# Kernel tuning notes

Measured on AMD Instinct MI355X. Metric: run time of the kernel, lower is better.

## Reference

```python
import jax, jax.numpy as jnp
import numpy as np

NUM_SEQS = 4
Q_LEN = 512          # new query tokens per sequence (chunked prefill)
SEQ_LEN = 2048       # total tokens per sequence (context + query)
NUM_Q_HEADS = 32
NUM_KV_HEADS = 8
HEAD_SIZE = 128
BLOCK_SIZE = 32
BLOCKS_PER_SEQ = SEQ_LEN // BLOCK_SIZE          # 64
NUM_BLOCKS = NUM_SEQS * BLOCKS_PER_SEQ          # 256 physical blocks


def setup_inputs() -> dict:
    key = jax.random.key(0)
    k1, k2, k3 = jax.random.split(key, 3)
    query = jax.random.normal(k1, (NUM_SEQS * Q_LEN, NUM_Q_HEADS, HEAD_SIZE), dtype=jnp.float32)
    key_cache = jax.random.normal(k2, (NUM_BLOCKS, BLOCK_SIZE, NUM_KV_HEADS, HEAD_SIZE), dtype=jnp.float32)
    value_cache = jax.random.normal(k3, (NUM_BLOCKS, BLOCK_SIZE, NUM_KV_HEADS, HEAD_SIZE), dtype=jnp.float32)
    # each sequence owns a contiguous run of physical blocks (any permutation works)
    block_tables = jnp.arange(NUM_BLOCKS, dtype=jnp.int32).reshape(NUM_SEQS, BLOCKS_PER_SEQ)
    seq_lens = jnp.full((NUM_SEQS,), SEQ_LEN, dtype=jnp.int32)
    query_start_loc = jnp.arange(NUM_SEQS + 1, dtype=jnp.int32) * Q_LEN
    return {"query": query, "key_cache": key_cache, "value_cache": value_cache,
            "block_tables": block_tables, "seq_lens": seq_lens,
            "query_start_loc": query_start_loc}


def reference(query, key_cache, value_cache, block_tables, seq_lens, query_start_loc):
    # paged/unified attention, base config: causal, GQA, no window/alibi/softcap/sinks/quant
    B, NB = block_tables.shape
    BS = key_cache.shape[1]
    total_q, Hq, D = query.shape
    Kvh = key_cache.shape[2]
    G = Hq // Kvh                       # num_queries_per_kv
    Lq = total_q // B                   # uniform query len per seq (matches query_start_loc)
    S = NB * BS                         # max kv length covered by block table
    scale = D ** -0.5

    q = query.reshape(B, Lq, Kvh, G, D)
    # gather paged KV: [B, NB, BS, Kvh, D] -> [B, S, Kvh, D]
    k = key_cache[block_tables].reshape(B, S, Kvh, D)
    v = value_cache[block_tables].reshape(B, S, Kvh, D)

    scores = jnp.einsum('blkgd,bskd->blkgs', q, k) * scale  # [B, Lq, Kvh, G, S]

    # absolute query positions: context_len + local pos, context_len = seq_len - Lq
    q_abs = (seq_lens - Lq)[:, None] + jnp.arange(Lq, dtype=seq_lens.dtype)[None, :]  # [B, Lq]
    kpos = jnp.arange(S, dtype=seq_lens.dtype)
    causal = kpos[None, None, :] <= q_abs[:, :, None]                 # key <= query pos
    valid = kpos[None, None, :] < seq_lens[:, None, None]             # key within seq
    mask = causal & valid                                             # [B, Lq, S]

    neg_inf = jnp.asarray(-jnp.inf, scores.dtype)
    scores = jnp.where(mask[:, :, None, None, :], scores, neg_inf)
    p = jax.nn.softmax(scores, axis=-1)
    out = jnp.einsum('blkgs,bskd->blkgd', p, v)                       # [B, Lq, Kvh, G, D]
    return out.reshape(total_q, Hq, D)
```

## Files before the change

### kernel.cpp

```cpp
#include <hip/hip_runtime.h>
#include <hip/hip_bf16.h>

typedef __bf16 bf16;
typedef __attribute__((ext_vector_type(8))) __bf16 bf16x8;
typedef __attribute__((ext_vector_type(4))) __bf16 bf16x4;
typedef __attribute__((ext_vector_type(4))) float f32x4;

static constexpr int NSEQ = 4;
static constexpr int LQ   = 512;
static constexpr int HQN  = 32;
static constexpr int HKVN = 8;
static constexpr int GQ   = 4;
static constexpr int DH   = 128;
static constexpr int BPS  = 64;
static constexpr int SKV  = 2048;
static constexpr int KVB  = 64;
static constexpr int QBL  = 32;

__device__ __forceinline__ bf16x8 cvt8(const float4& a, const float4& b) {
  bf16x8 o;
  o[0] = (bf16)a.x; o[1] = (bf16)a.y; o[2] = (bf16)a.z; o[3] = (bf16)a.w;
  o[4] = (bf16)b.x; o[5] = (bf16)b.y; o[6] = (bf16)b.z; o[7] = (bf16)b.w;
  return o;
}

__global__ void prep_k(const float* __restrict__ kc, const int* __restrict__ bt,
                       bf16* __restrict__ kb) {
  int e = (blockIdx.x * 256 + threadIdx.x) * 8;
  int d = e & 127;
  int s = (e >> 7) & 2047;
  int h = (e >> 18) & 7;
  int b = e >> 21;
  int pb = bt[b * BPS + (s >> 5)];
  const float* src = kc + (((size_t)pb * 32 + (s & 31)) * 8 + h) * 128 + d;
  float4 a = *(const float4*)src;
  float4 c = *(const float4*)(src + 4);
  *(bf16x8*)(kb + e) = cvt8(a, c);
}

__global__ void prep_vt(const float* __restrict__ vc, const int* __restrict__ bt,
                        bf16* __restrict__ vt) {
  __shared__ __align__(16) bf16 T[64][136];
  int bid = blockIdx.x;
  int st = bid & 31;
  int h  = (bid >> 5) & 7;
  int b  = bid >> 8;
  int tid = threadIdx.x;
  {
    int s  = tid >> 2;
    int d0 = (tid & 3) * 32;
    int sg = st * 64 + s;
    int pb = bt[b * BPS + (sg >> 5)];
    const float* src = vc + (((size_t)pb * 32 + (sg & 31)) * 8 + h) * 128 + d0;
#pragma unroll
    for (int k = 0; k < 4; ++k) {
      float4 a = *(const float4*)(src + 8 * k);
      float4 c = *(const float4*)(src + 8 * k + 4);
      *(bf16x8*)&T[s][d0 + 8 * k] = cvt8(a, c);
    }
  }
  __syncthreads();
  {
    int d  = tid & 127;
    int g2 = tid >> 7;
    bf16* dst = vt + (((size_t)(b * 8 + h)) * 128 + d) * SKV + st * 64 + g2 * 32;
#pragma unroll
    for (int k = 0; k < 4; ++k) {
      bf16x8 o;
#pragma unroll
      for (int j = 0; j < 8; ++j) o[j] = T[g2 * 32 + k * 8 + j][d];
      *(bf16x8*)(dst + 8 * k) = o;
    }
  }
}

template <bool WS>
__global__ __launch_bounds__(256, 2)
void attn_kern(const float* __restrict__ q, const float* __restrict__ kc,
               const float* __restrict__ vc, const int* __restrict__ bt,
               const int* __restrict__ seq_lens, const bf16* __restrict__ kb,
               const bf16* __restrict__ vtb, float* __restrict__ out) {
  __shared__ __align__(16) bf16 Kl[64][136];
  __shared__ __align__(16) bf16 Vl[128][72];
  __shared__ __align__(16) bf16 Pl[4][32][72];

  int bid = (int)blockIdx.x;
  int hi  = bid >> 8;
  int u   = bid & 255;
  int xcd = u & 7;
  int k2  = u >> 3;
  int c   = (k2 >> 3) | (xcd << 2);
  int i   = k2 & 7;
  int qt  = hi ? (15 - i) : i;
  int h   = c & 7;
  int b   = c >> 3;
  int lb  = qt * QBL;

  int tid  = (int)threadIdx.x;
  int w    = tid >> 6;
  int lane = tid & 63;
  int lq   = lane & 15;
  int lg   = lane >> 4;

  int ctx = seq_lens[b] - LQ;
  int nt  = (ctx + lb + QBL + KVB - 1) / KVB;

  const float CEXP = 0.08838834764831843f * 1.44269504088896340f;
  const float TH8  = 8.0f / CEXP;

  int hq = h * GQ + w;
  bf16x8 qf[2][4];
#pragma unroll
  for (int n = 0; n < 2; ++n) {
    const float* qp = q + (((size_t)(b * LQ + lb + n * 16 + lq)) * HQN + hq) * DH + lg * 8;
#pragma unroll
    for (int kk = 0; kk < 4; ++kk) {
      float4 a = *(const float4*)(qp + kk * 32);
      float4 c2 = *(const float4*)(qp + kk * 32 + 4);
      qf[n][kk] = cvt8(a, c2);
    }
  }

  f32x4 accO[2][8];
  f32x4 zero = {0.f, 0.f, 0.f, 0.f};
#pragma unroll
  for (int m = 0; m < 2; ++m)
#pragma unroll
    for (int nd = 0; nd < 8; ++nd) accO[m][nd] = zero;
  float mrun[2] = {-1e30f, -1e30f};
  float lrun[2] = {0.f, 0.f};

  const int* btr = bt + b * BPS;
  const bf16* kbase = WS ? kb  + (size_t)(b * 8 + h) * SKV * DH : nullptr;
  const bf16* vbase = WS ? vtb + (size_t)(b * 8 + h) * DH * SKV : nullptr;

  int ks_ = tid >> 2, kd0 = (tid & 3) * 32;
  int vd_ = tid >> 1, vs0 = (tid & 1) * 32;

  bf16x8 kpre[4], vpre[4];
  auto ldKV = [&](int t) {
    const bf16* ks = kbase + ((size_t)t * 64 + ks_) * DH + kd0;
#pragma unroll
    for (int k = 0; k < 4; ++k) kpre[k] = *(const bf16x8*)(ks + 8 * k);
    const bf16* vs = vbase + (size_t)vd_ * SKV + t * 64 + vs0;
#pragma unroll
    for (int k = 0; k < 4; ++k) vpre[k] = *(const bf16x8*)(vs + 8 * k);
  };
  auto stKV = [&]() {
#pragma unroll
    for (int k = 0; k < 4; ++k) *(bf16x8*)&Kl[ks_][kd0 + 8 * k] = kpre[k];
#pragma unroll
    for (int k = 0; k < 4; ++k) *(bf16x8*)&Vl[vd_][vs0 + 8 * k] = vpre[k];
  };

  auto compute = [&](int t) {
    f32x4 accS[4][2];
#pragma unroll
    for (int m = 0; m < 4; ++m)
#pragma unroll
      for (int n = 0; n < 2; ++n) accS[m][n] = zero;
#pragma unroll
    for (int m = 0; m < 4; ++m) {
      bf16x8 ak[4];
#pragma unroll
      for (int kk = 0; kk < 4; ++kk)
        ak[kk] = *(const bf16x8*)&Kl[m * 16 + lq][kk * 32 + lg * 8];
#pragma unroll
      for (int n = 0; n < 2; ++n)
#pragma unroll
        for (int kk = 0; kk < 4; ++kk)
          accS[m][n] = __builtin_amdgcn_mfma_f32_16x16x32_bf16(ak[kk], qf[n][kk], accS[m][n], 0, 0, 0);
    }

    if (t * KVB + KVB - 1 > ctx + lb) {
#pragma unroll
      for (int m = 0; m < 4; ++m) {
        int sg = t * 64 + m * 16 + lg * 4;
#pragma unroll
        for (int n = 0; n < 2; ++n) {
          int qpos = ctx + lb + n * 16 + lq;
#pragma unroll
          for (int r = 0; r < 4; ++r)
            if (sg + r > qpos) accS[m][n][r] = -1e30f;
        }
      }
    }

#pragma unroll
    for (int n = 0; n < 2; ++n) {
      float mx = accS[0][n][0];
#pragma unroll
      for (int m = 0; m < 4; ++m)
#pragma unroll
        for (int r = 0; r < 4; ++r) mx = fmaxf(mx, accS[m][n][r]);
      mx = fmaxf(mx, __shfl_xor(mx, 16));
      mx = fmaxf(mx, __shfl_xor(mx, 32));
      if (!__all(mx <= mrun[n] + TH8)) {
        float mnew = fmaxf(mrun[n], mx);
        float corr = exp2f((mrun[n] - mnew) * CEXP);
        mrun[n] = mnew;
        lrun[n] *= corr;
        float cb[4];
#pragma unroll
        for (int r = 0; r < 4; ++r) cb[r] = __shfl(corr, lg * 4 + r);
#pragma unroll
        for (int nd = 0; nd < 8; ++nd)
#pragma unroll
          for (int r = 0; r < 4; ++r) accO[n][nd][r] *= cb[r];
      }
      float psum = 0.f;
#pragma unroll
      for (int m = 0; m < 4; ++m) {
        bf16x4 pk;
#pragma unroll
        for (int r = 0; r < 4; ++r) {
          float p = exp2f((accS[m][n][r] - mrun[n]) * CEXP);
          psum += p;
          pk[r] = (bf16)p;
        }
        *(bf16x4*)&Pl[w][n * 16 + lq][m * 16 + lg * 4] = pk;
      }
      lrun[n] += psum;
    }

    asm volatile("s_waitcnt lgkmcnt(0)" ::: "memory");

    bf16x8 ap[2][2];
#pragma unroll
    for (int m2 = 0; m2 < 2; ++m2)
#pragma unroll
      for (int ks3 = 0; ks3 < 2; ++ks3)
        ap[m2][ks3] = *(const bf16x8*)&Pl[w][m2 * 16 + lq][ks3 * 32 + lg * 8];
#pragma unroll
    for (int nd = 0; nd < 8; ++nd) {
      bf16x8 bv0 = *(const bf16x8*)&Vl[nd * 16 + lq][lg * 8];
      bf16x8 bv1 = *(const bf16x8*)&Vl[nd * 16 + lq][32 + lg * 8];
#pragma unroll
      for (int m2 = 0; m2 < 2; ++m2) {
        accO[m2][nd] = __builtin_amdgcn_mfma_f32_16x16x32_bf16(ap[m2][0], bv0, accO[m2][nd], 0, 0, 0);
        accO[m2][nd] = __builtin_amdgcn_mfma_f32_16x16x32_bf16(ap[m2][1], bv1, accO[m2][nd], 0, 0, 0);
      }
    }
  };

  if (WS) {
    ldKV(0);
    stKV();
    __syncthreads();
    for (int t = 0; t < nt; ++t) {
      bool more = (t + 1 < nt);
      if (more) ldKV(t + 1);
      compute(t);
      if (more) {
        __syncthreads();
        stKV();
        __syncthreads();
      }
    }
  } else {
    for (int t = 0; t < nt; ++t) {
      {
        int s  = tid >> 2;
        int d0 = (tid & 3) * 32;
        int pb = btr[t * 2 + (s >> 5)];
        const float* ksrc = kc + (((size_t)pb * 32 + (s & 31)) * 8 + h) * 128 + d0;
#pragma unroll
        for (int k = 0; k < 4; ++k) {
          float4 a = *(const float4*)(ksrc + 8 * k);
          float4 c2 = *(const float4*)(ksrc + 8 * k + 4);
          *(bf16x8*)&Kl[s][d0 + 8 * k] = cvt8(a, c2);
        }
        int d  = tid & 127;
        int sh = tid >> 7;
        int pbv = btr[t * 2 + sh];
        const float* vsrc = vc + (((size_t)pbv * 32) * 8 + h) * 128 + d;
#pragma unroll
        for (int k = 0; k < 8; ++k) {
          bf16x4 o;
#pragma unroll
          for (int j = 0; j < 4; ++j) o[j] = (bf16)vsrc[(size_t)(k * 4 + j) * 1024];
          *(bf16x4*)&Vl[d][sh * 32 + 4 * k] = o;
        }
      }
      __syncthreads();
      compute(t);
      __syncthreads();
    }
  }

#pragma unroll
  for (int n = 0; n < 2; ++n) {
    lrun[n] += __shfl_xor(lrun[n], 16);
    lrun[n] += __shfl_xor(lrun[n], 32);
    lrun[n] = 1.f / lrun[n];
  }
#pragma unroll
  for (int m2 = 0; m2 < 2; ++m2) {
    float rb[4];
#pragma unroll
    for (int r = 0; r < 4; ++r) rb[r] = __shfl(lrun[m2], lg * 4 + r);
#pragma unroll
    for (int r = 0; r < 4; ++r) {
      float* op = out + (((size_t)(b * LQ + lb + m2 * 16 + lg * 4 + r)) * HQN + hq) * DH + lq;
#pragma unroll
      for (int nd = 0; nd < 8; ++nd) op[nd * 16] = accO[m2][nd][r] * rb[r];
    }
  }
}

extern "C" void kernel_launch(void* const* d_in, const int* in_sizes, int n_in,
                              void* d_out, int out_size, void* d_ws, size_t ws_size,
                              hipStream_t stream) {
  const float* q  = (const float*)d_in[0];
  const float* kc = (const float*)d_in[1];
  const float* vc = (const float*)d_in[2];
  const int* bt   = (const int*)d_in[3];
  const int* sl   = (const int*)d_in[4];
  float* out = (float*)d_out;

  size_t half = (size_t)NSEQ * HKVN * SKV * DH;
  size_t need = 2 * half * sizeof(bf16);
  if (ws_size >= need) {
    bf16* kb = (bf16*)d_ws;
    bf16* vt = kb + half;
    hipLaunchKernelGGL(prep_k, dim3(4096), dim3(256), 0, stream, kc, bt, kb);
    hipLaunchKernelGGL(prep_vt, dim3(1024), dim3(256), 0, stream, vc, bt, vt);
    hipLaunchKernelGGL((attn_kern<true>), dim3(512), dim3(256), 0, stream,
                       q, kc, vc, bt, sl, kb, vt, out);
  } else {
    hipLaunchKernelGGL((attn_kern<false>), dim3(512), dim3(256), 0, stream,
                       q, kc, vc, bt, sl, (const bf16*)nullptr, (const bf16*)nullptr, out);
  }
}
```

Measured before the change: 123.6 us.

## Feed P directly from registers into 16x16x16 MFMA, dropping LDS round-trip

```diff
diff --git a/kernel.cpp b/kernel.cpp
--- a/kernel.cpp
+++ b/kernel.cpp
@@ -5,6 +5,16 @@
 typedef __attribute__((ext_vector_type(8))) __bf16 bf16x8;
 typedef __attribute__((ext_vector_type(4))) __bf16 bf16x4;
 typedef __attribute__((ext_vector_type(4))) float f32x4;
+typedef __attribute__((ext_vector_type(4))) short s16x4;
+
+#if defined(__has_builtin)
+#  if __has_builtin(__builtin_amdgcn_mfma_f32_16x16x16bf16_1k)
+#    define HAVE_PV16 1
+#  endif
+#endif
+#ifndef HAVE_PV16
+#  define HAVE_PV16 0
+#endif
 
 static constexpr int NSEQ = 4;
 static constexpr int LQ   = 512;
@@ -75,14 +85,16 @@
 }
 
 template <bool WS>
-__global__ __launch_bounds__(256, 2)
+__global__ __launch_bounds__(256, HAVE_PV16 ? 3 : 2)
 void attn_kern(const float* __restrict__ q, const float* __restrict__ kc,
                const float* __restrict__ vc, const int* __restrict__ bt,
                const int* __restrict__ seq_lens, const bf16* __restrict__ kb,
                const bf16* __restrict__ vtb, float* __restrict__ out) {
   __shared__ __align__(16) bf16 Kl[64][136];
   __shared__ __align__(16) bf16 Vl[128][72];
+#if !HAVE_PV16
   __shared__ __align__(16) bf16 Pl[4][32][72];
+#endif
 
   int bid = (int)blockIdx.x;
   int hi  = bid >> 8;
@@ -210,21 +222,53 @@
       }
       float psum = 0.f;
 #pragma unroll
-      for (int m = 0; m < 4; ++m) {
-        bf16x4 pk;
+      for (int m = 0; m < 4; ++m)
 #pragma unroll
         for (int r = 0; r < 4; ++r) {
           float p = exp2f((accS[m][n][r] - mrun[n]) * CEXP);
           psum += p;
-          pk[r] = (bf16)p;
+          accS[m][n][r] = p;
         }
+      lrun[n] += psum;
+    }
+
+#if HAVE_PV16
+    bf16x4 pa[4][2];
+#pragma unroll
+    for (int m = 0; m < 4; ++m)
+#pragma unroll
+      for (int n = 0; n < 2; ++n) {
+        bf16x4 t4;
+#pragma unroll
+        for (int e = 0; e < 4; ++e) t4[e] = (bf16)accS[m][n][e];
+        pa[m][n] = t4;
+      }
+
+#pragma unroll
+    for (int nd = 0; nd < 8; ++nd) {
+      bf16x4 bv[4];
+#pragma unroll
+      for (int m = 0; m < 4; ++m)
+        bv[m] = *(const bf16x4*)&Vl[nd * 16 + lq][m * 16 + lg * 4];
+#pragma unroll
+      for (int m = 0; m < 4; ++m)
+#pragma unroll
+        for (int n = 0; n < 2; ++n)
+          accO[n][nd] = __builtin_amdgcn_mfma_f32_16x16x16bf16_1k(
+              __builtin_bit_cast(s16x4, pa[m][n]),
+              __builtin_bit_cast(s16x4, bv[m]), accO[n][nd], 0, 0, 0);
+    }
+#else
+#pragma unroll
+    for (int n = 0; n < 2; ++n)
+#pragma unroll
+      for (int m = 0; m < 4; ++m) {
+        bf16x4 pk;
+#pragma unroll
+        for (int r = 0; r < 4; ++r) pk[r] = (bf16)accS[m][n][r];
         *(bf16x4*)&Pl[w][n * 16 + lq][m * 16 + lg * 4] = pk;
       }
-      lrun[n] += psum;
-    }
-
     asm volatile("s_waitcnt lgkmcnt(0)" ::: "memory");
-
     bf16x8 ap[2][2];
 #pragma unroll
     for (int m2 = 0; m2 < 2; ++m2)
@@ -241,6 +285,7 @@
         accO[m2][nd] = __builtin_amdgcn_mfma_f32_16x16x32_bf16(ap[m2][1], bv1, accO[m2][nd], 0, 0, 0);
       }
     }
+#endif
   };
 
   if (WS) {
```

After: 217.6 us. +76.1%, slower.

## Halve query tile to 16 rows, double grid, keep P in registers

Applied to the files above, without the earlier changes.

```diff
diff --git a/kernel.cpp b/kernel.cpp
--- a/kernel.cpp
+++ b/kernel.cpp
@@ -5,6 +5,16 @@
 typedef __attribute__((ext_vector_type(8))) __bf16 bf16x8;
 typedef __attribute__((ext_vector_type(4))) __bf16 bf16x4;
 typedef __attribute__((ext_vector_type(4))) float f32x4;
+typedef __attribute__((ext_vector_type(4))) short s16x4;
+
+#if defined(__has_builtin)
+#  if __has_builtin(__builtin_amdgcn_mfma_f32_16x16x16bf16_1k)
+#    define HAVE_PV16 1
+#  endif
+#endif
+#ifndef HAVE_PV16
+#  define HAVE_PV16 0
+#endif
 
 static constexpr int NSEQ = 4;
 static constexpr int LQ   = 512;
@@ -15,7 +25,7 @@
 static constexpr int BPS  = 64;
 static constexpr int SKV  = 2048;
 static constexpr int KVB  = 64;
-static constexpr int QBL  = 32;
+static constexpr int QBL  = 16;
 
 __device__ __forceinline__ bf16x8 cvt8(const float4& a, const float4& b) {
   bf16x8 o;
@@ -75,23 +85,25 @@
 }
 
 template <bool WS>
-__global__ __launch_bounds__(256, 2)
+__global__ __launch_bounds__(256, 4)
 void attn_kern(const float* __restrict__ q, const float* __restrict__ kc,
                const float* __restrict__ vc, const int* __restrict__ bt,
                const int* __restrict__ seq_lens, const bf16* __restrict__ kb,
                const bf16* __restrict__ vtb, float* __restrict__ out) {
   __shared__ __align__(16) bf16 Kl[64][136];
   __shared__ __align__(16) bf16 Vl[128][72];
-  __shared__ __align__(16) bf16 Pl[4][32][72];
+#if !HAVE_PV16
+  __shared__ __align__(16) bf16 Pl[4][16][72];
+#endif
 
   int bid = (int)blockIdx.x;
-  int hi  = bid >> 8;
-  int u   = bid & 255;
+  int hi  = bid >> 9;
+  int u   = bid & 511;
   int xcd = u & 7;
   int k2  = u >> 3;
-  int c   = (k2 >> 3) | (xcd << 2);
-  int i   = k2 & 7;
-  int qt  = hi ? (15 - i) : i;
+  int c   = (k2 & 3) | (xcd << 2);
+  int i   = k2 >> 2;
+  int qt  = hi ? (31 - i) : i;
   int h   = c & 7;
   int b   = c >> 3;
   int lb  = qt * QBL;
@@ -104,31 +116,29 @@
 
   int ctx = seq_lens[b] - LQ;
   int nt  = (ctx + lb + QBL + KVB - 1) / KVB;
+  int qpos = ctx + lb + lq;
 
   const float CEXP = 0.08838834764831843f * 1.44269504088896340f;
   const float TH8  = 8.0f / CEXP;
 
   int hq = h * GQ + w;
-  bf16x8 qf[2][4];
-#pragma unroll
-  for (int n = 0; n < 2; ++n) {
-    const float* qp = q + (((size_t)(b * LQ + lb + n * 16 + lq)) * HQN + hq) * DH + lg * 8;
+  bf16x8 qf[4];
+  {
+    const float* qp = q + (((size_t)(b * LQ + lb + lq)) * HQN + hq) * DH + lg * 8;
 #pragma unroll
     for (int kk = 0; kk < 4; ++kk) {
       float4 a = *(const float4*)(qp + kk * 32);
       float4 c2 = *(const float4*)(qp + kk * 32 + 4);
-      qf[n][kk] = cvt8(a, c2);
-    }
-  }
-
-  f32x4 accO[2][8];
+      qf[kk] = cvt8(a, c2);
+    }
+  }
+
+  f32x4 accO[8];
   f32x4 zero = {0.f, 0.f, 0.f, 0.f};
 #pragma unroll
-  for (int m = 0; m < 2; ++m)
-#pragma unroll
-    for (int nd = 0; nd < 8; ++nd) accO[m][nd] = zero;
-  float mrun[2] = {-1e30f, -1e30f};
-  float lrun[2] = {0.f, 0.f};
+  for (int nd = 0; nd < 8; ++nd) accO[nd] = zero;
+  float mrun = -1e30f;
+  float lrun = 0.f;
 
   const int* btr = bt + b * BPS;
   const bf16* kbase = WS ? kb  + (size_t)(b * 8 + h) * SKV * DH : nullptr;
@@ -154,93 +164,103 @@
   };
 
   auto compute = [&](int t) {
-    f32x4 accS[4][2];
-#pragma unroll
-    for (int m = 0; m < 4; ++m)
-#pragma unroll
-      for (int n = 0; n < 2; ++n) accS[m][n] = zero;
+    f32x4 accS[4];
+#pragma unroll
+    for (int m = 0; m < 4; ++m) accS[m] = zero;
+    __builtin_amdgcn_s_setprio(1);
 #pragma unroll
     for (int m = 0; m < 4; ++m) {
-      bf16x8 ak[4];
-#pragma unroll
-      for (int kk = 0; kk < 4; ++kk)
-        ak[kk] = *(const bf16x8*)&Kl[m * 16 + lq][kk * 32 + lg * 8];
-#pragma unroll
-      for (int n = 0; n < 2; ++n)
-#pragma unroll
-        for (int kk = 0; kk < 4; ++kk)
-          accS[m][n] = __builtin_amdgcn_mfma_f32_16x16x32_bf16(ak[kk], qf[n][kk], accS[m][n], 0, 0, 0);
-    }
+#pragma unroll
+      for (int kk = 0; kk < 4; ++kk) {
+        bf16x8 ak = *(const bf16x8*)&Kl[m * 16 + lq][kk * 32 + lg * 8];
+        accS[m] = __builtin_amdgcn_mfma_f32_16x16x32_bf16(ak, qf[kk], accS[m], 0, 0, 0);
+      }
+    }
+    __builtin_amdgcn_s_setprio(0);
 
     if (t * KVB + KVB - 1 > ctx + lb) {
 #pragma unroll
       for (int m = 0; m < 4; ++m) {
         int sg = t * 64 + m * 16 + lg * 4;
 #pragma unroll
-        for (int n = 0; n < 2; ++n) {
-          int qpos = ctx + lb + n * 16 + lq;
-#pragma unroll
-          for (int r = 0; r < 4; ++r)
-            if (sg + r > qpos) accS[m][n][r] = -1e30f;
-        }
-      }
-    }
-
-#pragma unroll
-    for (int n = 0; n < 2; ++n) {
-      float mx = accS[0][n][0];
+        for (int r = 0; r < 4; ++r)
+          if (sg + r > qpos) accS[m][r] = -1e30f;
+      }
+    }
+
+    {
+      float mx = accS[0][0];
 #pragma unroll
       for (int m = 0; m < 4; ++m)
 #pragma unroll
-        for (int r = 0; r < 4; ++r) mx = fmaxf(mx, accS[m][n][r]);
+        for (int r = 0; r < 4; ++r) mx = fmaxf(mx, accS[m][r]);
       mx = fmaxf(mx, __shfl_xor(mx, 16));
       mx = fmaxf(mx, __shfl_xor(mx, 32));
-      if (!__all(mx <= mrun[n] + TH8)) {
-        float mnew = fmaxf(mrun[n], mx);
-        float corr = exp2f((mrun[n] - mnew) * CEXP);
-        mrun[n] = mnew;
-        lrun[n] *= corr;
+      if (!__all(mx <= mrun + TH8)) {
+        float mnew = fmaxf(mrun, mx);
+        float corr = exp2f((mrun - mnew) * CEXP);
+        mrun = mnew;
+        lrun *= corr;
         float cb[4];
 #pragma unroll
         for (int r = 0; r < 4; ++r) cb[r] = __shfl(corr, lg * 4 + r);
 #pragma unroll
         for (int nd = 0; nd < 8; ++nd)
 #pragma unroll
-          for (int r = 0; r < 4; ++r) accO[n][nd][r] *= cb[r];
+          for (int r = 0; r < 4; ++r) accO[nd][r] *= cb[r];
       }
       float psum = 0.f;
 #pragma unroll
+      for (int m = 0; m < 4; ++m)
+#pragma unroll
+        for (int r = 0; r < 4; ++r) {
+          float p = exp2f((accS[m][r] - mrun) * CEXP);
+          psum += p;
+          accS[m][r] = p;
+        }
+      lrun += psum;
+    }
+
+#if HAVE_PV16
+    bf16x4 pa[4];
+#pragma unroll
+    for (int m = 0; m < 4; ++m)
+#pragma unroll
+      for (int e = 0; e < 4; ++e) pa[m][e] = (bf16)accS[m][e];
+
+    __builtin_amdgcn_s_setprio(1);
+#pragma unroll
+    for (int nd = 0; nd < 8; ++nd) {
+#pragma unroll
       for (int m = 0; m < 4; ++m) {
-        bf16x4 pk;
-#pragma unroll
-        for (int r = 0; r < 4; ++r) {
-          float p = exp2f((accS[m][n][r] - mrun[n]) * CEXP);
-          psum += p;
-          pk[r] = (bf16)p;
-        }
-        *(bf16x4*)&Pl[w][n * 16 + lq][m * 16 + lg * 4] = pk;
-      }
-      lrun[n] += psum;
-    }
-
+        bf16x4 bv = *(const bf16x4*)&Vl[nd * 16 + lq][m * 16 + lg * 4];
+        accO[nd] = __builtin_amdgcn_mfma_f32_16x16x16bf16_1k(
+            __builtin_bit_cast(s16x4, pa[m]),
+            __builtin_bit_cast(s16x4, bv), accO[nd], 0, 0, 0);
+      }
+    }
+    __builtin_amdgcn_s_setprio(0);
+#else
+#pragma unroll
+    for (int m = 0; m < 4; ++m) {
+      bf16x4 pk;
+#pragma unroll
+      for (int r = 0; r < 4; ++r) pk[r] = (bf16)accS[m][r];
+      *(bf16x4*)&Pl[w][lq][m * 16 + lg * 4] = pk;
+    }
     asm volatile("s_waitcnt lgkmcnt(0)" ::: "memory");
-
-    bf16x8 ap[2][2];
-#pragma unroll
-    for (int m2 = 0; m2 < 2; ++m2)
-#pragma unroll
-      for (int ks3 = 0; ks3 < 2; ++ks3)
-        ap[m2][ks3] = *(const bf16x8*)&Pl[w][m2 * 16 + lq][ks3 * 32 + lg * 8];
+    bf16x8 ap[2];
+#pragma unroll
+    for (int ks3 = 0; ks3 < 2; ++ks3)
+      ap[ks3] = *(const bf16x8*)&Pl[w][lq][ks3 * 32 + lg * 8];
 #pragma unroll
     for (int nd = 0; nd < 8; ++nd) {
       bf16x8 bv0 = *(const bf16x8*)&Vl[nd * 16 + lq][lg * 8];
       bf16x8 bv1 = *(const bf16x8*)&Vl[nd * 16 + lq][32 + lg * 8];
-#pragma unroll
-      for (int m2 = 0; m2 < 2; ++m2) {
-        accO[m2][nd] = __builtin_amdgcn_mfma_f32_16x16x32_bf16(ap[m2][0], bv0, accO[m2][nd], 0, 0, 0);
-        accO[m2][nd] = __builtin_amdgcn_mfma_f32_16x16x32_bf16(ap[m2][1], bv1, accO[m2][nd], 0, 0, 0);
-      }
-    }
+      accO[nd] = __builtin_amdgcn_mfma_f32_16x16x32_bf16(ap[0], bv0, accO[nd], 0, 0, 0);
+      accO[nd] = __builtin_amdgcn_mfma_f32_16x16x32_bf16(ap[1], bv1, accO[nd], 0, 0, 0);
+    }
+#endif
   };
 
   if (WS) {
@@ -288,23 +308,17 @@
     }
   }
 
-#pragma unroll
-  for (int n = 0; n < 2; ++n) {
-    lrun[n] += __shfl_xor(lrun[n], 16);
-    lrun[n] += __shfl_xor(lrun[n], 32);
-    lrun[n] = 1.f / lrun[n];
-  }
-#pragma unroll
-  for (int m2 = 0; m2 < 2; ++m2) {
-    float rb[4];
-#pragma unroll
-    for (int r = 0; r < 4; ++r) rb[r] = __shfl(lrun[m2], lg * 4 + r);
-#pragma unroll
-    for (int r = 0; r < 4; ++r) {
-      float* op = out + (((size_t)(b * LQ + lb + m2 * 16 + lg * 4 + r)) * HQN + hq) * DH + lq;
-#pragma unroll
-      for (int nd = 0; nd < 8; ++nd) op[nd * 16] = accO[m2][nd][r] * rb[r];
-    }
+  lrun += __shfl_xor(lrun, 16);
+  lrun += __shfl_xor(lrun, 32);
+  float linv = 1.f / lrun;
+  float rb[4];
+#pragma unroll
+  for (int r = 0; r < 4; ++r) rb[r] = __shfl(linv, lg * 4 + r);
+#pragma unroll
+  for (int r = 0; r < 4; ++r) {
+    float* op = out + (((size_t)(b * LQ + lb + lg * 4 + r)) * HQN + hq) * DH + lq;
+#pragma unroll
+    for (int nd = 0; nd < 8; ++nd) op[nd * 16] = accO[nd][r] * rb[r];
   }
 }
 
@@ -325,10 +339,10 @@
     bf16* vt = kb + half;
     hipLaunchKernelGGL(prep_k, dim3(4096), dim3(256), 0, stream, kc, bt, kb);
     hipLaunchKernelGGL(prep_vt, dim3(1024), dim3(256), 0, stream, vc, bt, vt);
-    hipLaunchKernelGGL((attn_kern<true>), dim3(512), dim3(256), 0, stream,
+    hipLaunchKernelGGL((attn_kern<true>), dim3(1024), dim3(256), 0, stream,
                        q, kc, vc, bt, sl, kb, vt, out);
   } else {
-    hipLaunchKernelGGL((attn_kern<false>), dim3(512), dim3(256), 0, stream,
+    hipLaunchKernelGGL((attn_kern<false>), dim3(1024), dim3(256), 0, stream,
                        q, kc, vc, bt, sl, (const bf16*)nullptr, (const bf16*)nullptr, out);
   }
 }
```

After: 148.7 us. 1.2x slower.
